# Performance work log

Hardware: AMD Instinct MI355X
Metric: run time of the kernel (lower is better)

## Reference

```python
import jax, jax.numpy as jnp
import numpy as np

NUM_SLOTS = 64
MEMORY_DIM = 512
EMBED_DIM = 1024
SCALE = MEMORY_DIM ** (-0.5)


def setup_inputs() -> dict:
    key = jax.random.key(0)
    ks = jax.random.split(key, 7)
    B, S, E, Dm = 8, 4096, EMBED_DIM, MEMORY_DIM
    s = 0.02
    return {
        "embeddings": jax.random.normal(ks[0], (B, S, E), dtype=jnp.float32),
        "W_write": jax.random.normal(ks[1], (E, Dm), dtype=jnp.float32) * s,
        "b_write": jnp.zeros((Dm,), dtype=jnp.float32),
        "W_query": jax.random.normal(ks[2], (E, Dm), dtype=jnp.float32) * s,
        "b_query": jnp.zeros((Dm,), dtype=jnp.float32),
        "W_out": jax.random.normal(ks[3], (Dm, E), dtype=jnp.float32) * s,
        "b_out": jnp.zeros((E,), dtype=jnp.float32),
    }


def reference(embeddings, W_write, b_write, W_query, b_query, W_out, b_out):
    B, S, E = embeddings.shape
    M, Dm = NUM_SLOTS, MEMORY_DIM
    # Precompute per-token projections (linear, so identical to per-step).
    write_vals = jnp.einsum('bse,ed->bsd', embeddings, W_write) + b_write  # [B,S,Dm]
    queries = jnp.einsum('bse,ed->bsd', embeddings, W_query) + b_query      # [B,S,Dm]
    addrs = jnp.arange(S) % M  # hash(position) = position % M

    def step(carry, xs):
        memory, written = carry            # [B,M,Dm], [B,M] bool
        q, wv, addr = xs                   # [B,Dm], [B,Dm], scalar int
        # read BEFORE write (current token not yet in memory)
        sim = jnp.einsum('bd,bmd->bm', q, memory) * SCALE
        sim = jnp.where(written, sim, -jnp.inf)
        attn = jax.nn.softmax(sim, axis=-1)
        attn = jnp.nan_to_num(attn)        # all-unwritten -> zeros
        retrieved = jnp.einsum('bm,bmd->bd', attn, memory)
        memory = memory.at[:, addr, :].set(wv)
        written = written.at[:, addr].set(True)
        return (memory, written), retrieved

    mem0 = jnp.zeros((B, M, Dm), dtype=embeddings.dtype)
    wr0 = jnp.zeros((B, M), dtype=bool)
    xs = (queries.transpose(1, 0, 2), write_vals.transpose(1, 0, 2), addrs)
    _, retrieved = jax.lax.scan(step, (mem0, wr0), xs)  # [S,B,Dm]
    retrieved = retrieved.transpose(1, 0, 2)            # [B,S,Dm]
    # read_out is linear per-step -> apply once over the whole sequence
    return jnp.einsum('bsd,de->bse', retrieved, W_out) + b_out
```

## Files before the change

kernel.cpp:

```cpp
#include <hip/hip_runtime.h>
#include <hip/hip_bf16.h>
#include <math.h>


#define BATCH   8
#define S_LEN   4096
#define EMB     1024
#define DM      512
#define MROWS   (BATCH * S_LEN)
#define SCALE_F 0.04419417382415922f

typedef __attribute__((ext_vector_type(4))) float f32x4;
typedef __attribute__((ext_vector_type(8))) short short8;

__device__ __forceinline__ unsigned short f2bf(float f) {
    __hip_bfloat16 h = __float2bfloat16(f);
    return *reinterpret_cast<unsigned short*>(&h);
}

__global__ __launch_bounds__(256) void cast_bf16(const float4* __restrict__ in,
                                                 ushort4* __restrict__ out, int n4)
{
    int id = blockIdx.x * 256 + threadIdx.x;
    if (id >= n4) return;
    float4 v = in[id];
    ushort4 o;
    o.x = f2bf(v.x); o.y = f2bf(v.y); o.z = f2bf(v.z); o.w = f2bf(v.w);
    out[id] = o;
}

__global__ __launch_bounds__(256) void tcast(const float* __restrict__ in,
                                             __hip_bfloat16* __restrict__ out,
                                             int K, int N)
{
    int id = blockIdx.x * 256 + threadIdx.x;
    if (id >= K * N) return;
    int n = id / K, k = id % K;
    out[id] = __float2bfloat16(in[k * N + n]);
}

__global__ __launch_bounds__(256) void concat_bias(const float* __restrict__ a,
                                                   const float* __restrict__ b,
                                                   float* __restrict__ out)
{
    int i = blockIdx.x * 256 + threadIdx.x;
    if (i < 512) out[i] = a[i];
    else if (i < 1024) out[i] = b[i - 512];
}

template<bool BF16OUT>
__global__ __launch_bounds__(512, 2) void gemm256(
    const __hip_bfloat16* __restrict__ A, int lda,
    const __hip_bfloat16* __restrict__ Bt, int ldb,
    const float* __restrict__ bias,
    void* __restrict__ Cv, int ldc,
    int K, int nbx)
{
    __shared__ __align__(16) char smem[131072];

    const int nwg = gridDim.x;
    const int bid = blockIdx.x;
    const int cpx = nwg >> 3;
    const int swz = (bid & 7) * cpx + (bid >> 3);
    const int bm0 = (swz / nbx) << 8;
    const int bn0 = (swz % nbx) << 8;

    const int tid  = threadIdx.x;
    const int lane = tid & 63;
    const int w    = tid >> 6;
    const int wm   = w >> 2, wn = w & 3;
    const int l15  = lane & 15, lhi = lane >> 4;
    const int nt   = K >> 6;

    const int srow  = w * 8 + (lane >> 3);
    const int scol8 = (((lane & 7) ^ (lane >> 3)) << 3);

    auto stage_tile = [&](int buf, int kt) {
#pragma unroll
        for (int h = 0; h < 4; ++h) {
            const int isB = h >> 1, hh = h & 1;
            const __hip_bfloat16* G = isB ? Bt : A;
            const int ldg = isB ? ldb : lda;
            const int rb  = (isB ? bn0 : bm0) + hh * 128;
#pragma unroll
            for (int i = 0; i < 2; ++i) {
                const __hip_bfloat16* g =
                    G + (size_t)(rb + i * 64 + srow) * ldg + kt + scol8;
                char* l = smem + buf * 65536 + isB * 32768 + hh * 16384
                          + i * 8192 + w * 1024;
                __builtin_amdgcn_global_load_lds(
                    (const __attribute__((address_space(1))) unsigned int*)g,
                    (__attribute__((address_space(3))) unsigned int*)l, 16, 0, 0);
            }
        }
    };

    f32x4 acc[8][4] = {};

    stage_tile(0, 0);
    __syncthreads();

    for (int t = 0; t < nt; ++t) {
        const int cur = t & 1;
        if (t + 1 < nt) stage_tile(cur ^ 1, (t + 1) << 6);

        const char* sA = smem + cur * 65536;
        const char* sB = sA + 32768;

#pragma unroll
        for (int q = 0; q < 4; ++q) {
            const int mh = q >> 1, nh = q & 1;
            short8 af[4][2], bfv[2][2];
#pragma unroll
            for (int mi = 0; mi < 4; ++mi) {
                const int r = wm * 128 + mh * 64 + mi * 16 + l15;
#pragma unroll
                for (int kk = 0; kk < 2; ++kk) {
                    const int pc = (kk * 4 + lhi) ^ (r & 7);
                    af[mi][kk] = *(const short8*)(sA + r * 128 + (pc << 4));
                }
            }
#pragma unroll
            for (int ni = 0; ni < 2; ++ni) {
                const int r = wn * 64 + nh * 32 + ni * 16 + l15;
#pragma unroll
                for (int kk = 0; kk < 2; ++kk) {
                    const int pc = (kk * 4 + lhi) ^ (r & 7);
                    bfv[ni][kk] = *(const short8*)(sB + r * 128 + (pc << 4));
                }
            }
#pragma unroll
            for (int mi = 0; mi < 4; ++mi)
#pragma unroll
                for (int ni = 0; ni < 2; ++ni)
#pragma unroll
                    for (int kk = 0; kk < 2; ++kk)
                        acc[mh * 4 + mi][nh * 2 + ni] =
                            __builtin_amdgcn_mfma_f32_16x16x32_bf16(
                                af[mi][kk], bfv[ni][kk],
                                acc[mh * 4 + mi][nh * 2 + ni], 0, 0, 0);
        }
        __syncthreads();
    }

    float bv[4];
#pragma unroll
    for (int N = 0; N < 4; ++N)
        bv[N] = bias[bn0 + wn * 64 + (N >> 1) * 32 + (N & 1) * 16 + l15];

#pragma unroll
    for (int M = 0; M < 8; ++M)
#pragma unroll
        for (int N = 0; N < 4; ++N)
#pragma unroll
            for (int reg = 0; reg < 4; ++reg) {
                int row = bm0 + wm * 128 + (M >> 2) * 64 + (M & 3) * 16
                          + lhi * 4 + reg;
                int col = bn0 + wn * 64 + (N >> 1) * 32 + (N & 1) * 16 + l15;
                float v = acc[M][N][reg] + bv[N];
                if (BF16OUT)
                    ((__hip_bfloat16*)Cv)[(size_t)row * ldc + col] = __float2bfloat16(v);
                else
                    ((float*)Cv)[(size_t)row * ldc + col] = v;
            }
}

__global__ __launch_bounds__(256) void transpose_wv(
    const unsigned short* __restrict__ wvq,
    unsigned short* __restrict__ wvt)
{
    __shared__ unsigned short tl[64][66];
    const int tx  = blockIdx.x;
    const int dx  = blockIdx.y;
    const int b   = blockIdx.z;
    const int tid = threadIdx.x;
    const int r   = tid >> 3;
    const int c8  = (tid & 7) * 8;
    const size_t bbase = (size_t)b << 12;

#pragma unroll
    for (int it = 0; it < 2; ++it) {
        int row = r + it * 32;
        uint4 v = *(const uint4*)(wvq + ((bbase + tx * 64 + row) << 10) + dx * 64 + c8);
        *(unsigned*)&tl[row][c8 + 0] = v.x;
        *(unsigned*)&tl[row][c8 + 2] = v.y;
        *(unsigned*)&tl[row][c8 + 4] = v.z;
        *(unsigned*)&tl[row][c8 + 6] = v.w;
    }
    __syncthreads();
#pragma unroll
    for (int it = 0; it < 2; ++it) {
        int drow = r + it * 32;
        union { unsigned short s[8]; uint4 v; } o;
#pragma unroll
        for (int k = 0; k < 8; ++k) o.s[k] = tl[c8 + k][drow];
        *(uint4*)(wvt + (((size_t)b * 512 + dx * 64 + drow) << 12) + tx * 64 + c8) = o.v;
    }
}

__global__ __launch_bounds__(256) void attn_mfma(
    const __hip_bfloat16* __restrict__ WVQ,
    const __hip_bfloat16* __restrict__ WVT,
    __hip_bfloat16* __restrict__ R)
{
    __shared__ __align__(16) unsigned short p_lds[64][136];

    const int blk = blockIdx.x;
    const int b   = blk >> 6;
    const int t0  = (blk & 63) << 6;
    const int jmin = (t0 == 0) ? 64 : 0;
    const size_t bbase = (size_t)b << 12;
    const int tid  = threadIdx.x;
    const int lane = tid & 63;
    const int w    = tid >> 6;
    const int l15  = lane & 15;
    const int lhi  = lane >> 4;

    f32x4 acc[8] = {};
    const __hip_bfloat16* q0 =
        WVQ + ((bbase + t0 + w * 16 + l15) << 10) + 512 + lhi * 8;

    const __hip_bfloat16* brow[8];
#pragma unroll
    for (int nt = 0; nt < 8; ++nt) {
        int aj = t0 - 64 + nt * 16 + l15;
        if (aj < 0) aj = 0;
        brow[nt] = WVQ + ((bbase + aj) << 10) + lhi * 8;
    }

    for (int kt = 0; kt < 16; ++kt) {
        short8 qa = *(const short8*)(q0 + kt * 32);
#pragma unroll
        for (int nt = 0; nt < 8; ++nt) {
            short8 bv = *(const short8*)(brow[nt] + kt * 32);
            acc[nt] = __builtin_amdgcn_mfma_f32_16x16x32_bf16(qa, bv, acc[nt], 0, 0, 0);
        }
    }

    float m4[4] = { -1e30f, -1e30f, -1e30f, -1e30f };
#pragma unroll
    for (int nt = 0; nt < 8; ++nt)
#pragma unroll
        for (int reg = 0; reg < 4; ++reg) {
            int i = w * 16 + lhi * 4 + reg;
            int j = nt * 16 + l15;
            bool valid = (j >= i) && (j <= i + 63) && (j >= jmin);
            float s = valid ? acc[nt][reg] * SCALE_F : -1e30f;
            acc[nt][reg] = s;
            m4[reg] = fmaxf(m4[reg], s);
        }
#pragma unroll
    for (int off = 8; off >= 1; off >>= 1)
#pragma unroll
        for (int reg = 0; reg < 4; ++reg)
            m4[reg] = fmaxf(m4[reg], __shfl_xor(m4[reg], off, 64));

    float sum4[4] = {};
#pragma unroll
    for (int nt = 0; nt < 8; ++nt)
#pragma unroll
        for (int reg = 0; reg < 4; ++reg) {
            float s = acc[nt][reg];
            float p = (s > -1e29f) ? __expf(s - m4[reg]) : 0.f;
            acc[nt][reg] = p;
            sum4[reg] += p;
        }
#pragma unroll
    for (int off = 8; off >= 1; off >>= 1)
#pragma unroll
        for (int reg = 0; reg < 4; ++reg)
            sum4[reg] += __shfl_xor(sum4[reg], off, 64);

    float rs4[4];
#pragma unroll
    for (int reg = 0; reg < 4; ++reg)
        rs4[reg] = (sum4[reg] > 0.f) ? 1.f / sum4[reg] : 0.f;

#pragma unroll
    for (int nt = 0; nt < 8; ++nt)
#pragma unroll
        for (int reg = 0; reg < 4; ++reg)
            p_lds[w * 16 + lhi * 4 + reg][nt * 16 + l15] =
                f2bf(acc[nt][reg] * rs4[reg]);

    __syncthreads();

    short8 pa[4];
#pragma unroll
    for (int kt = 0; kt < 4; ++kt)
        pa[kt] = *(const short8*)&p_lds[w * 16 + l15][kt * 32 + lhi * 8];

    int tclamp[4];
#pragma unroll
    for (int kt = 0; kt < 4; ++kt) {
        int ti = t0 - 64 + kt * 32 + lhi * 8;
        tclamp[kt] = ti < 0 ? 0 : ti;
    }

    const size_t vbase = (size_t)b * 512;
    for (int nt = 0; nt < 32; ++nt) {
        int d = nt * 16 + l15;
        f32x4 a = {};
#pragma unroll
        for (int kt = 0; kt < 4; ++kt) {
            short8 bv = *(const short8*)(WVT + ((vbase + d) << 12) + tclamp[kt]);
            a = __builtin_amdgcn_mfma_f32_16x16x32_bf16(pa[kt], bv, a, 0, 0, 0);
        }
        size_t rb = (bbase + t0 + w * 16 + lhi * 4) << 9;
#pragma unroll
        for (int reg = 0; reg < 4; ++reg)
            R[rb + ((size_t)reg << 9) + d] = __float2bfloat16(a[reg]);
    }
}

extern "C" void kernel_launch(void* const* d_in, const int* in_sizes, int n_in,
                              void* d_out, int out_size, void* d_ws, size_t ws_size,
                              hipStream_t stream)
{
    const float* emb   = (const float*)d_in[0];
    const float* W_wr  = (const float*)d_in[1];
    const float* b_wr  = (const float*)d_in[2];
    const float* W_qr  = (const float*)d_in[3];
    const float* b_qr  = (const float*)d_in[4];
    const float* W_out = (const float*)d_in[5];
    const float* b_out = (const float*)d_in[6];
    float* out = (float*)d_out;

    char* ws = (char*)d_ws;
    __hip_bfloat16* embb = (__hip_bfloat16*)(ws);
    __hip_bfloat16* wvt  = (__hip_bfloat16*)(ws);
    __hip_bfloat16* wvq  = (__hip_bfloat16*)(ws + (((size_t)64) << 20));
    __hip_bfloat16* rbuf = (__hip_bfloat16*)(ws + (((size_t)128) << 20));
    __hip_bfloat16* wcat = (__hip_bfloat16*)(ws + (((size_t)160) << 20));
    __hip_bfloat16* wout = (__hip_bfloat16*)(ws + (((size_t)162) << 20));
    float*          bcat = (float*)        (ws + (((size_t)163) << 20));

    cast_bf16<<<dim3((MROWS * EMB / 4) / 256), dim3(256), 0, stream>>>(
        (const float4*)emb, (ushort4*)embb, MROWS * EMB / 4);
    tcast<<<dim3(2048), dim3(256), 0, stream>>>(W_wr, wcat, EMB, DM);
    tcast<<<dim3(2048), dim3(256), 0, stream>>>(W_qr, wcat + (size_t)DM * EMB, EMB, DM);
    tcast<<<dim3(2048), dim3(256), 0, stream>>>(W_out, wout, DM, EMB);
    concat_bias<<<dim3(4), dim3(256), 0, stream>>>(b_wr, b_qr, bcat);

    gemm256<true><<<dim3(512), dim3(512), 0, stream>>>(
        embb, EMB, wcat, EMB, bcat, (void*)wvq, 1024, EMB, 4);

    transpose_wv<<<dim3(64, 8, 8), dim3(256), 0, stream>>>(
        (const unsigned short*)wvq, (unsigned short*)wvt);

    attn_mfma<<<dim3(MROWS / 64), dim3(256), 0, stream>>>(wvq, wvt, rbuf);

    gemm256<false><<<dim3(512), dim3(512), 0, stream>>>(
        rbuf, DM, wout, DM, b_out, (void*)out, EMB, DM, 4);
}
```

Before: 250.6 us.

## Merge prep kernels into one launch and restructure GEMM fragment loads

Five small preprocessing launches (embedding cast, three weight transposes, bias concat) are folded into a single kernel that dispatches on block index. In the GEMM, the B fragments are loaded once per k-tile instead of being reloaded for each quarter, and the trailing barrier is skipped on the last iteration. The staging row/column mapping is rewritten in terms of thread id. Partial unrolling pragmas are added to two loops in the attention kernel. Holding all B fragments at once raises register pressure in a kernel already limited by launch bounds of 512 threads with 2 blocks.

```diff
diff --git a/kernel.cpp b/kernel.cpp
--- a/kernel.cpp
+++ b/kernel.cpp
@@ -18,34 +18,39 @@
     return *reinterpret_cast<unsigned short*>(&h);
 }
 
-__global__ __launch_bounds__(256) void cast_bf16(const float4* __restrict__ in,
-                                                 ushort4* __restrict__ out, int n4)
-{
-    int id = blockIdx.x * 256 + threadIdx.x;
-    if (id >= n4) return;
-    float4 v = in[id];
-    ushort4 o;
-    o.x = f2bf(v.x); o.y = f2bf(v.y); o.z = f2bf(v.z); o.w = f2bf(v.w);
-    out[id] = o;
-}
-
-__global__ __launch_bounds__(256) void tcast(const float* __restrict__ in,
-                                             __hip_bfloat16* __restrict__ out,
-                                             int K, int N)
-{
-    int id = blockIdx.x * 256 + threadIdx.x;
-    if (id >= K * N) return;
-    int n = id / K, k = id % K;
-    out[id] = __float2bfloat16(in[k * N + n]);
-}
-
-__global__ __launch_bounds__(256) void concat_bias(const float* __restrict__ a,
-                                                   const float* __restrict__ b,
-                                                   float* __restrict__ out)
-{
-    int i = blockIdx.x * 256 + threadIdx.x;
-    if (i < 512) out[i] = a[i];
-    else if (i < 1024) out[i] = b[i - 512];
+__global__ __launch_bounds__(256) void prep(
+    const float4* __restrict__ emb4, ushort4* __restrict__ embb4,
+    const float* __restrict__ W_wr, const float* __restrict__ W_qr,
+    const float* __restrict__ W_out,
+    const float* __restrict__ b_wr, const float* __restrict__ b_qr,
+    __hip_bfloat16* __restrict__ wcat, __hip_bfloat16* __restrict__ wout,
+    float* __restrict__ bcat)
+{
+    const int bx = blockIdx.x;
+    if (bx < 32768) {
+        int id = bx * 256 + threadIdx.x;
+        float4 v = emb4[id];
+        ushort4 o;
+        o.x = f2bf(v.x); o.y = f2bf(v.y); o.z = f2bf(v.z); o.w = f2bf(v.w);
+        embb4[id] = o;
+    } else if (bx < 32768 + 2048) {
+        int id = (bx - 32768) * 256 + threadIdx.x;
+        int n = id >> 10, k = id & 1023;
+        wcat[id] = __float2bfloat16(W_wr[k * 512 + n]);
+    } else if (bx < 32768 + 4096) {
+        int id = (bx - 32768 - 2048) * 256 + threadIdx.x;
+        int n = id >> 10, k = id & 1023;
+        wcat[(size_t)DM * EMB + id] = __float2bfloat16(W_qr[k * 512 + n]);
+    } else if (bx < 32768 + 6144) {
+        int id = (bx - 32768 - 4096) * 256 + threadIdx.x;
+        int n = id >> 9, k = id & 511;
+        wout[id] = __float2bfloat16(W_out[k * 1024 + n]);
+    } else {
+        int i = threadIdx.x;
+#pragma unroll
+        for (int r = 0; r < 4; ++r, i += 256)
+            bcat[i] = (i < 512) ? b_wr[i] : b_qr[i - 512];
+    }
 }
 
 template<bool BF16OUT>
@@ -72,8 +77,8 @@
     const int l15  = lane & 15, lhi = lane >> 4;
     const int nt   = K >> 6;
 
-    const int srow  = w * 8 + (lane >> 3);
-    const int scol8 = (((lane & 7) ^ (lane >> 3)) << 3);
+    const int r64 = tid >> 3;
+    const int cg8 = ((tid & 7) ^ (r64 & 7)) << 3;
 
     auto stage_tile = [&](int buf, int kt) {
 #pragma unroll
@@ -85,7 +90,7 @@
 #pragma unroll
             for (int i = 0; i < 2; ++i) {
                 const __hip_bfloat16* g =
-                    G + (size_t)(rb + i * 64 + srow) * ldg + kt + scol8;
+                    G + (size_t)(rb + i * 64 + r64) * ldg + kt + cg8;
                 char* l = smem + buf * 65536 + isB * 32768 + hh * 16384
                           + i * 8192 + w * 1024;
                 __builtin_amdgcn_global_load_lds(
@@ -102,15 +107,28 @@
 
     for (int t = 0; t < nt; ++t) {
         const int cur = t & 1;
-        if (t + 1 < nt) stage_tile(cur ^ 1, (t + 1) << 6);
+        const bool pf = (t + 1 < nt);
+        if (pf) stage_tile(cur ^ 1, (t + 1) << 6);
 
         const char* sA = smem + cur * 65536;
         const char* sB = sA + 32768;
 
-#pragma unroll
-        for (int q = 0; q < 4; ++q) {
-            const int mh = q >> 1, nh = q & 1;
-            short8 af[4][2], bfv[2][2];
+        short8 bfv[2][2][2];
+#pragma unroll
+        for (int nh = 0; nh < 2; ++nh)
+#pragma unroll
+            for (int ni = 0; ni < 2; ++ni) {
+                const int r = wn * 64 + nh * 32 + ni * 16 + l15;
+#pragma unroll
+                for (int kk = 0; kk < 2; ++kk) {
+                    const int pc = (kk * 4 + lhi) ^ (r & 7);
+                    bfv[nh][ni][kk] = *(const short8*)(sB + r * 128 + (pc << 4));
+                }
+            }
+
+#pragma unroll
+        for (int mh = 0; mh < 2; ++mh) {
+            short8 af[4][2];
 #pragma unroll
             for (int mi = 0; mi < 4; ++mi) {
                 const int r = wm * 128 + mh * 64 + mi * 16 + l15;
@@ -121,26 +139,20 @@
                 }
             }
 #pragma unroll
-            for (int ni = 0; ni < 2; ++ni) {
-                const int r = wn * 64 + nh * 32 + ni * 16 + l15;
-#pragma unroll
-                for (int kk = 0; kk < 2; ++kk) {
-                    const int pc = (kk * 4 + lhi) ^ (r & 7);
-                    bfv[ni][kk] = *(const short8*)(sB + r * 128 + (pc << 4));
-                }
-            }
-#pragma unroll
-            for (int mi = 0; mi < 4; ++mi)
-#pragma unroll
-                for (int ni = 0; ni < 2; ++ni)
-#pragma unroll
-                    for (int kk = 0; kk < 2; ++kk)
-                        acc[mh * 4 + mi][nh * 2 + ni] =
-                            __builtin_amdgcn_mfma_f32_16x16x32_bf16(
-                                af[mi][kk], bfv[ni][kk],
-                                acc[mh * 4 + mi][nh * 2 + ni], 0, 0, 0);
-        }
-        __syncthreads();
+            for (int nh = 0; nh < 2; ++nh)
+#pragma unroll
+                for (int mi = 0; mi < 4; ++mi)
+#pragma unroll
+                    for (int ni = 0; ni < 2; ++ni)
+#pragma unroll
+                        for (int kk = 0; kk < 2; ++kk)
+                            acc[mh * 4 + mi][nh * 2 + ni] =
+                                __builtin_amdgcn_mfma_f32_16x16x32_bf16(
+                                    af[mi][kk], bfv[nh][ni][kk],
+                                    acc[mh * 4 + mi][nh * 2 + ni], 0, 0, 0);
+        }
+
+        if (pf) __syncthreads();
     }
 
     float bv[4];
@@ -228,6 +240,7 @@
         brow[nt] = WVQ + ((bbase + aj) << 10) + lhi * 8;
     }
 
+#pragma unroll 2
     for (int kt = 0; kt < 16; ++kt) {
         short8 qa = *(const short8*)(q0 + kt * 32);
 #pragma unroll
@@ -298,6 +311,7 @@
     }
 
     const size_t vbase = (size_t)b * 512;
+#pragma unroll 2
     for (int nt = 0; nt < 32; ++nt) {
         int d = nt * 16 + l15;
         f32x4 a = {};
@@ -335,12 +349,9 @@
     __hip_bfloat16* wout = (__hip_bfloat16*)(ws + (((size_t)162) << 20));
     float*          bcat = (float*)        (ws + (((size_t)163) << 20));
 
-    cast_bf16<<<dim3((MROWS * EMB / 4) / 256), dim3(256), 0, stream>>>(
-        (const float4*)emb, (ushort4*)embb, MROWS * EMB / 4);
-    tcast<<<dim3(2048), dim3(256), 0, stream>>>(W_wr, wcat, EMB, DM);
-    tcast<<<dim3(2048), dim3(256), 0, stream>>>(W_qr, wcat + (size_t)DM * EMB, EMB, DM);
-    tcast<<<dim3(2048), dim3(256), 0, stream>>>(W_out, wout, DM, EMB);
-    concat_bias<<<dim3(4), dim3(256), 0, stream>>>(b_wr, b_qr, bcat);
+    prep<<<dim3(38913), dim3(256), 0, stream>>>(
+        (const float4*)emb, (ushort4*)embb,
+        W_wr, W_qr, W_out, b_wr, b_qr, wcat, wout, bcat);
 
     gemm256<true><<<dim3(512), dim3(512), 0, stream>>>(
         embb, EMB, wcat, EMB, bcat, (void*)wvq, 1024, EMB, 4);
```

After: 238.2 us. 1.05x faster.
